# Kernel optimization log

Hardware: AMD Instinct MI355X
Metric: run time of the kernel (lower is better)

The kernel has to match this reference:

```python
import jax, jax.numpy as jnp
import numpy as np

HIDDEN_DIM = 256
NLAT, NLON = 64, 128
BATCH, N_STATIONS = 2, 1024


def _grid_coords():
    lat = jnp.linspace(-90.0, 90.0, NLAT)
    lon = jnp.linspace(-180.0, 180.0, NLON)
    lat_mesh, lon_mesh = jnp.meshgrid(lat, lon, indexing='ij')
    return lat_mesh.reshape(-1), lon_mesh.reshape(-1)  # (n_grid,)


def setup_inputs() -> dict:
    key = jax.random.key(0)
    k1, k2, k3, k4, k5, k6 = jax.random.split(key, 6)
    station_features = jax.random.normal(k1, (BATCH, N_STATIONS, HIDDEN_DIM), dtype=jnp.float32)
    station_coords = jax.random.normal(k2, (BATCH, N_STATIONS, 3), dtype=jnp.float32)
    mask = jnp.ones((BATCH, N_STATIONS), dtype=jnp.float32)
    # distance_mlp params: Linear(3,32) -> GELU -> Linear(32,1) -> Softplus
    W1 = jax.random.normal(k3, (3, 32), dtype=jnp.float32) * (1.0 / np.sqrt(3.0))
    b1 = jax.random.normal(k4, (32,), dtype=jnp.float32) * 0.02
    W2 = jax.random.normal(k5, (32, 1), dtype=jnp.float32) * (1.0 / np.sqrt(32.0))
    b2 = jax.random.normal(k6, (1,), dtype=jnp.float32) * 0.02
    return {"station_features": station_features, "station_coords": station_coords,
            "mask": mask, "W1": W1, "b1": b1, "W2": W2, "b2": b2}


def reference(station_features, station_coords, mask, W1, b1, W2, b2):
    lat_grid, lon_grid = _grid_coords()  # (G,)
    station_lat = station_coords[:, :, 0]  # (B,S)
    station_lon = station_coords[:, :, 1]
    dlat = station_lat[:, :, None] - lat_grid[None, None, :]  # (B,S,G)
    dlon = station_lon[:, :, None] - lon_grid[None, None, :]
    dist = jnp.sqrt(dlat**2 + dlon**2 + 1e-6)
    dist_features = jnp.stack([dist, dlat, dlon], axis=-1)  # (B,S,G,3)
    h = jax.nn.gelu(dist_features @ W1 + b1, approximate=False)  # (B,S,G,32)
    weights = jax.nn.softplus((h @ W2 + b2)[..., 0])  # (B,S,G)
    weights = weights * mask[:, :, None]
    weights = jax.nn.softmax(weights, axis=1)  # over stations
    grid = jnp.einsum('bsg,bsd->bgd', weights, station_features)
    grid = grid.reshape(station_features.shape[0], NLAT, NLON, HIDDEN_DIM)
    return jnp.transpose(grid, (0, 3, 1, 2))  # (B, D, nlat, nlon)
```

## Files before the change

kernel.cpp:

```cpp
#include <hip/hip_runtime.h>
#include <math.h>

#define NLAT 64
#define NLON 128
#define HID  256
#define NSTA 1024
#define TG   16
#define SC   128
#define NCHUNK (NSTA / SC)
#define NGRP 16

#define LOG2E 1.4426950408889634f
#define LN2   0.69314718055994531f
#define GA (-2.3022082f)
#define GB (-0.1029432f)

typedef float f32x4 __attribute__((ext_vector_type(4)));
typedef _Float16 f16x8 __attribute__((ext_vector_type(8)));

__global__ __launch_bounds__(256)
void cvt_kernel(const float* __restrict__ feats, _Float16* __restrict__ fhi,
                _Float16* __restrict__ flo) {
    __shared__ float tile[64][65];
    const int blk = blockIdx.x;
    const int b  = blk >> 6;
    const int st = (blk >> 2) & 15;
    const int dt = blk & 3;
    const int x = threadIdx.x & 63, y = threadIdx.x >> 6;
#pragma unroll 4
    for (int k = 0; k < 16; ++k) {
        int s = k * 4 + y;
        tile[s][x] = feats[((size_t)(b * NSTA + st * 64 + s)) * HID + dt * 64 + x];
    }
    __syncthreads();
#pragma unroll 4
    for (int k = 0; k < 16; ++k) {
        int dl = k * 4 + y;
        float v = tile[x][dl];
        _Float16 hi = (_Float16)v;
        _Float16 lo = (_Float16)(v - (float)hi);
        size_t o = ((size_t)(b * HID + dt * 64 + dl)) * NSTA + st * 64 + x;
        fhi[o] = hi;
        flo[o] = lo;
    }
}

__global__ __launch_bounds__(256, 4)
void s2g_kernel(const float* __restrict__ coords,
                const float* __restrict__ maskp,
                const float* __restrict__ W1,
                const float* __restrict__ b1,
                const float* __restrict__ W2,
                const float* __restrict__ b2p,
                const _Float16* __restrict__ fhi,
                const _Float16* __restrict__ flo,
                float* __restrict__ out)
{
    __shared__ __align__(16) f16x8 fragAh[256];
    __shared__ __align__(16) f16x8 fragAl[256];
    __shared__ __align__(16) float slat[SC], slon[SC], smask[SC];
    __shared__ float4 wpack[32];
    __shared__ float w2s[32];
    __shared__ __align__(16) float maxbuf[NGRP * TG], psum[NGRP * TG];
    __shared__ __align__(16) float mS[TG], lS[TG], alphaS[TG];

    const int tid  = threadIdx.x;
    const int blk  = blockIdx.x & 511;
    const int b    = blockIdx.x >> 9;
    const int lat  = blk >> 3;
    const int lon0 = (blk & 7) * TG;

    const float latv = -90.0f + (180.0f / 63.0f) * (float)lat;

    if (tid < 32) {
        wpack[tid] = make_float4(W1[tid], W1[32 + tid], W1[64 + tid], b1[tid]);
        w2s[tid]   = W2[tid];
        if (tid < TG) { mS[tid] = -1.0e30f; lS[tid] = 0.0f; }
    }
    const float b2 = b2p[0];

    const int gA   = tid & (TG - 1);
    const int sgrp = tid >> 4;
    const float lonvA = -180.0f + (360.0f / 127.0f) * (float)(lon0 + gA);

    const int lane = tid & 63;
    const int wv   = tid >> 6;

    f32x4 acc[4];
#pragma unroll
    for (int t = 0; t < 4; ++t) acc[t] = (f32x4){0.0f, 0.0f, 0.0f, 0.0f};

    const float* cbase = coords + (size_t)b * NSTA * 3;
    const float* mbase = maskp  + (size_t)b * NSTA;
    const _Float16* fhb = fhi + (size_t)b * HID * NSTA;
    const _Float16* flb = flo + (size_t)b * HID * NSTA;

    for (int c = 0; c < NCHUNK; ++c) {
        const int s0 = c * SC;
        __syncthreads();
        if (tid < SC) {
            slat[tid]  = cbase[(size_t)(s0 + tid) * 3 + 0];
            slon[tid]  = cbase[(size_t)(s0 + tid) * 3 + 1];
            smask[tid] = mbase[s0 + tid];
        }
        __syncthreads();

        float dist[8], dlat[8], dlon[8], v[8];
#pragma unroll
        for (int i = 0; i < 8; ++i) {
            int s = sgrp * 8 + i;
            float dla = slat[s] - latv;
            float dlo = slon[s] - lonvA;
            dlat[i] = dla;
            dlon[i] = dlo;
            dist[i] = sqrtf(fmaf(dla, dla, fmaf(dlo, dlo, 1e-6f)));
            v[i] = b2;
        }
#pragma unroll 2
        for (int j = 0; j < 32; ++j) {
            float4 wj = wpack[j];
            float  w2 = w2s[j];
#pragma unroll
            for (int i = 0; i < 8; ++i) {
                float pre  = fmaf(wj.x, dist[i], fmaf(wj.y, dlat[i], fmaf(wj.z, dlon[i], wj.w)));
                float t    = pre * pre;
                float earg = fmaf(GB, t, GA) * pre;
                float e    = __builtin_amdgcn_exp2f(earg);
                float r    = __builtin_amdgcn_rcpf(1.0f + e);
                v[i] = fmaf(w2 * pre, r, v[i]);
            }
        }
        float lmax = -3.0e38f;
#pragma unroll
        for (int i = 0; i < 8; ++i) {
            int s = sgrp * 8 + i;
            float x  = v[i];
            float ax = fabsf(x);
            float e  = __builtin_amdgcn_exp2f(-ax * LOG2E);
            float sp = fmaxf(x, 0.0f) + __builtin_amdgcn_logf(1.0f + e) * LN2;
            v[i] = sp * smask[s];
            lmax = fmaxf(lmax, v[i]);
        }
        maxbuf[sgrp * TG + gA] = lmax;
        __syncthreads();

        if (tid < TG) {
            float cm = maxbuf[tid];
#pragma unroll
            for (int k = 1; k < NGRP; ++k) cm = fmaxf(cm, maxbuf[k * TG + tid]);
            float mold = mS[tid];
            float mnew = fmaxf(mold, cm);
            alphaS[tid] = __builtin_amdgcn_exp2f((mold - mnew) * LOG2E);
            mS[tid] = mnew;
        }
        __syncthreads();

        {
            float m  = mS[gA];
            float ps = 0.0f;
            f16x8 fh, fl;
#pragma unroll
            for (int i = 0; i < 8; ++i) {
                float p = __builtin_amdgcn_exp2f((v[i] - m) * LOG2E);
                _Float16 h = (_Float16)p;
                fh[i] = h;
                fl[i] = (_Float16)(p - (float)h);
                ps += p;
            }
            const int idx = ((sgrp >> 2) << 6) + (((sgrp & 3) << 4) | gA);
            fragAh[idx] = fh;
            fragAl[idx] = fl;
            psum[sgrp * TG + gA] = ps;
        }
        __syncthreads();

        if (tid < TG) {
            float t = 0.0f;
#pragma unroll
            for (int k = 0; k < NGRP; ++k) t += psum[k * TG + tid];
            lS[tid] = lS[tid] * alphaS[tid] + t;
        }

        {
            const f32x4 al = *(const f32x4*)&alphaS[(lane >> 4) * 4];
#pragma unroll
            for (int t = 0; t < 4; ++t) acc[t] = acc[t] * al;

            const int srow = s0 + ((lane >> 4) * 8);
            const int dbase = wv * 64 + (lane & 15);
#pragma unroll
            for (int kc = 0; kc < 4; ++kc) {
                f16x8 ah = fragAh[(kc << 6) + lane];
                f16x8 al16 = fragAl[(kc << 6) + lane];
#pragma unroll
                for (int t = 0; t < 4; ++t) {
                    const size_t off = (size_t)(dbase + t * 16) * NSTA + srow + kc * 32;
                    f16x8 bh = *(const f16x8*)(fhb + off);
                    f16x8 bl = *(const f16x8*)(flb + off);
                    acc[t] = __builtin_amdgcn_mfma_f32_16x16x32_f16(ah, bh, acc[t], 0, 0, 0);
                    acc[t] = __builtin_amdgcn_mfma_f32_16x16x32_f16(ah, bl, acc[t], 0, 0, 0);
                    acc[t] = __builtin_amdgcn_mfma_f32_16x16x32_f16(al16, bh, acc[t], 0, 0, 0);
                }
            }
        }
    }
    __syncthreads();

    {
        const float4 l4 = *(const float4*)&lS[(lane >> 4) * 4];
        const float4 rl = make_float4(1.0f / l4.x, 1.0f / l4.y, 1.0f / l4.z, 1.0f / l4.w);
        const int m0 = (lane >> 4) * 4;
        const size_t gbase = (size_t)lat * NLON + lon0 + m0;
#pragma unroll
        for (int t = 0; t < 4; ++t) {
            const int d = wv * 64 + t * 16 + (lane & 15);
            float4 o;
            o.x = acc[t].x * rl.x;
            o.y = acc[t].y * rl.y;
            o.z = acc[t].z * rl.z;
            o.w = acc[t].w * rl.w;
            *reinterpret_cast<float4*>(out + ((size_t)(b * HID + d)) * (NLAT * NLON) + gbase) = o;
        }
    }
}

extern "C" void kernel_launch(void* const* d_in, const int* in_sizes, int n_in,
                              void* d_out, int out_size, void* d_ws, size_t ws_size,
                              hipStream_t stream) {
    const float* feats  = (const float*)d_in[0];
    const float* coords = (const float*)d_in[1];
    const float* maskp  = (const float*)d_in[2];
    const float* W1     = (const float*)d_in[3];
    const float* b1     = (const float*)d_in[4];
    const float* W2     = (const float*)d_in[5];
    const float* b2     = (const float*)d_in[6];
    float* out          = (float*)d_out;

    _Float16* fhi = (_Float16*)d_ws;
    _Float16* flo = fhi + (size_t)2 * HID * NSTA;

    hipLaunchKernelGGL(cvt_kernel, dim3(128), dim3(256), 0, stream, feats, fhi, flo);
    hipLaunchKernelGGL(s2g_kernel, dim3(1024), dim3(256), 0, stream,
                       coords, maskp, W1, b1, W2, b2, fhi, flo, out);
}
```

Measured before the change: 283.1 us.

## Replace GELU evaluation with shared-memory lookup table and vectorize conversion kernel

The per-element GELU in the distance MLP is now computed as relu(x) plus a correction read from a 4096-entry shared-memory table, built per block with an erf approximation and covering [-4.5, 4.5]. This swaps an exp and a reciprocal per element for a clamp, an index calculation and an LDS gather. The gather can hit bank conflicts, and each block pays to build the table. Nearest-entry lookup without interpolation adds error compared with the earlier sigmoid-based approximation. The fp16 split conversion kernel is also reworked to use float4 loads and 4-wide half stores over 512 smaller blocks.

```diff
diff --git a/kernel.cpp b/kernel.cpp
--- a/kernel.cpp
+++ b/kernel.cpp
@@ -9,40 +9,60 @@
 #define SC   128
 #define NCHUNK (NSTA / SC)
 #define NGRP 16
+#define TABN 4096
+#define TABW 4.5f
 
 #define LOG2E 1.4426950408889634f
 #define LN2   0.69314718055994531f
-#define GA (-2.3022082f)
-#define GB (-0.1029432f)
 
 typedef float f32x4 __attribute__((ext_vector_type(4)));
 typedef _Float16 f16x8 __attribute__((ext_vector_type(8)));
+typedef _Float16 f16x4 __attribute__((ext_vector_type(4)));
+
+__device__ __forceinline__ float gelu_ref(float x) {
+    const float p  = 0.3275911f;
+    const float a1 = 0.254829592f, a2 = -0.284496736f, a3 = 1.421413741f,
+                a4 = -1.453152027f, a5 = 1.061405429f;
+    float z  = x * 0.70710678118654752f;
+    float az = fabsf(z);
+    float t  = __builtin_amdgcn_rcpf(fmaf(p, az, 1.0f));
+    float poly = fmaf(fmaf(fmaf(fmaf(a5, t, a4), t, a3), t, a2), t, a1) * t;
+    float e  = __builtin_amdgcn_exp2f(az * az * -LOG2E);
+    float r  = fmaf(-poly, e, 1.0f);
+    float erfz = copysignf(r, z);
+    float hx = 0.5f * x;
+    return fmaf(hx, erfz, hx);
+}
 
 __global__ __launch_bounds__(256)
 void cvt_kernel(const float* __restrict__ feats, _Float16* __restrict__ fhi,
                 _Float16* __restrict__ flo) {
-    __shared__ float tile[64][65];
+    __shared__ float tile[16][64];
     const int blk = blockIdx.x;
-    const int b  = blk >> 6;
-    const int st = (blk >> 2) & 15;
+    const int b  = blk >> 8;
+    const int st = (blk >> 2) & 63;
     const int dt = blk & 3;
-    const int x = threadIdx.x & 63, y = threadIdx.x >> 6;
-#pragma unroll 4
-    for (int k = 0; k < 16; ++k) {
-        int s = k * 4 + y;
-        tile[s][x] = feats[((size_t)(b * NSTA + st * 64 + s)) * HID + dt * 64 + x];
+    {
+        const int s  = threadIdx.x >> 4;
+        const int dq = threadIdx.x & 15;
+        const float4 vv = *(const float4*)
+            &feats[((size_t)(b * NSTA + st * 16 + s)) * HID + dt * 64 + dq * 4];
+        *(float4*)&tile[s][dq * 4] = vv;
     }
     __syncthreads();
-#pragma unroll 4
-    for (int k = 0; k < 16; ++k) {
-        int dl = k * 4 + y;
-        float v = tile[x][dl];
-        _Float16 hi = (_Float16)v;
-        _Float16 lo = (_Float16)(v - (float)hi);
-        size_t o = ((size_t)(b * HID + dt * 64 + dl)) * NSTA + st * 64 + x;
-        fhi[o] = hi;
-        flo[o] = lo;
-    }
+    const int d  = threadIdx.x >> 2;
+    const int sq = threadIdx.x & 3;
+    f16x4 hi4, lo4;
+#pragma unroll
+    for (int k = 0; k < 4; ++k) {
+        float v = tile[sq * 4 + k][d];
+        _Float16 h = (_Float16)v;
+        hi4[k] = h;
+        lo4[k] = (_Float16)(v - (float)h);
+    }
+    const size_t o = ((size_t)(b * HID + dt * 64 + d)) * NSTA + st * 16 + sq * 4;
+    *(f16x4*)&fhi[o] = hi4;
+    *(f16x4*)&flo[o] = lo4;
 }
 
 __global__ __launch_bounds__(256, 4)
@@ -56,6 +76,7 @@
                 const _Float16* __restrict__ flo,
                 float* __restrict__ out)
 {
+    __shared__ float gtab[TABN];
     __shared__ __align__(16) f16x8 fragAh[256];
     __shared__ __align__(16) f16x8 fragAl[256];
     __shared__ __align__(16) float slat[SC], slon[SC], smask[SC];
@@ -72,6 +93,12 @@
 
     const float latv = -90.0f + (180.0f / 63.0f) * (float)lat;
 
+    const float TH = 2.0f * TABW / (float)TABN;
+#pragma unroll
+    for (int k = tid; k < TABN; k += 256) {
+        float x = -TABW + ((float)k + 0.5f) * TH;
+        gtab[k] = gelu_ref(x) - fmaxf(x, 0.0f);
+    }
     if (tid < 32) {
         wpack[tid] = make_float4(W1[tid], W1[32 + tid], W1[64 + tid], b1[tid]);
         w2s[tid]   = W2[tid];
@@ -94,6 +121,9 @@
     const float* mbase = maskp  + (size_t)b * NSTA;
     const _Float16* fhb = fhi + (size_t)b * HID * NSTA;
     const _Float16* flb = flo + (size_t)b * HID * NSTA;
+
+    const float ISCALE = (float)TABN / (2.0f * TABW);
+    const float IOFF   = (float)TABN * 0.5f;
 
     for (int c = 0; c < NCHUNK; ++c) {
         const int s0 = c * SC;
@@ -122,12 +152,12 @@
             float  w2 = w2s[j];
 #pragma unroll
             for (int i = 0; i < 8; ++i) {
-                float pre  = fmaf(wj.x, dist[i], fmaf(wj.y, dlat[i], fmaf(wj.z, dlon[i], wj.w)));
-                float t    = pre * pre;
-                float earg = fmaf(GB, t, GA) * pre;
-                float e    = __builtin_amdgcn_exp2f(earg);
-                float r    = __builtin_amdgcn_rcpf(1.0f + e);
-                v[i] = fmaf(w2 * pre, r, v[i]);
+                float pre = fmaf(wj.x, dist[i], fmaf(wj.y, dlat[i], fmaf(wj.z, dlon[i], wj.w)));
+                float cl  = fminf(fmaxf(pre, -TABW), 4.4999f);
+                int  idx  = (int)fmaf(cl, ISCALE, IOFF);
+                float r   = gtab[idx];
+                v[i] = fmaf(w2, fmaxf(pre, 0.0f), v[i]);
+                v[i] = fmaf(w2, r, v[i]);
             }
         }
         float lmax = -3.0e38f;
@@ -239,7 +269,7 @@
     _Float16* fhi = (_Float16*)d_ws;
     _Float16* flo = fhi + (size_t)2 * HID * NSTA;
 
-    hipLaunchKernelGGL(cvt_kernel, dim3(128), dim3(256), 0, stream, feats, fhi, flo);
+    hipLaunchKernelGGL(cvt_kernel, dim3(512), dim3(256), 0, stream, feats, fhi, flo);
     hipLaunchKernelGGL(s2g_kernel, dim3(1024), dim3(256), 0, stream,
                        coords, maskp, W1, b1, W2, b2, fhi, flo, out);
 }
```

After: 248.0 us. 12.4% less time.
